# Optimization experiments

Hardware: AMD Instinct MI355X
Metric: run time of the kernel (lower is better)

## Reference

```python
import jax, jax.numpy as jnp
import numpy as np

HEAD_NUM = 16

def setup_inputs() -> dict:
    key = jax.random.key(0)
    k1, k2 = jax.random.split(key)
    bs, seq, d = 2, 2048, 1024
    embeddings = jax.random.normal(k1, (bs, seq, d), dtype=jnp.float32)
    W = jax.random.normal(k2, (d, 3 * d), dtype=jnp.float32) * (1.0 / np.sqrt(d))
    b = jnp.zeros((3 * d,), dtype=jnp.float32)
    return {"embeddings": embeddings, "W": W, "b": b}

def reference(embeddings, W, b):
    bs, seq, d = embeddings.shape
    h = HEAD_NUM
    qkv = embeddings @ W + b                      # [b, s, 3d]
    q, k, v = jnp.split(qkv, 3, axis=-1)          # each [b, s, d]
    hd = d // h
    # Faithful to source: reshape to (bs, seq, head_dim, heads) then permute
    def split_heads(x, head_dim):
        return x.reshape(bs, seq, head_dim, h).transpose(0, 3, 1, 2)  # [b, h, s, hd]
    mq = split_heads(q, hd)
    mk = split_heads(k, hd)
    mv = split_heads(v, hd)
    scale = jnp.sqrt(jnp.asarray(hd, dtype=mq.dtype))
    scores = jnp.einsum('bhqd,bhkd->bhqk', mq, mk) / scale  # [b, h, s, s]
    attn = jax.nn.softmax(scores, axis=-1)
    out = jnp.einsum('bhqk,bhkv->bhqv', attn, mv)            # [b, h, s, hd]
    return out.transpose(0, 2, 1, 3).reshape(bs, seq, -1)    # [b, s, d]
```

## Files before the change

### kernel.cpp

```cpp
#include <hip/hip_runtime.h>
#include <stdint.h>

typedef unsigned short u16;
typedef unsigned int u32;
typedef unsigned int u32x2 __attribute__((ext_vector_type(2)));
typedef float f32x4 __attribute__((ext_vector_type(4)));
typedef __bf16 bf16x8 __attribute__((ext_vector_type(8)));

#define BS 2
#define SEQ 2048
#define DIM 1024
#define NW3 3072
#define NH 16
#define HD 64

#define MFMA_BF16(a, b, c) __builtin_amdgcn_mfma_f32_16x16x32_bf16((a), (b), (c), 0, 0, 0)

#define GLL16(g, l)                                                                \
  __builtin_amdgcn_global_load_lds(                                                \
      (__attribute__((address_space(1))) void*)(void*)(uintptr_t)(g),              \
      (__attribute__((address_space(3))) void*)(l), 16, 0, 0)

__device__ __forceinline__ float fexp2(float x) {
#if defined(__has_builtin)
#if __has_builtin(__builtin_amdgcn_exp2f)
  return __builtin_amdgcn_exp2f(x);
#else
  return exp2f(x);
#endif
#else
  return exp2f(x);
#endif
}

__device__ __forceinline__ u16 f2bf(float x) {
  __bf16 h = (__bf16)x;
  return __builtin_bit_cast(u16, h);
}

#define CSC 0.18033688011112042f

#if defined(__has_builtin)
#if __has_builtin(__builtin_amdgcn_permlane32_swap) && \
    __has_builtin(__builtin_amdgcn_permlane16_swap)
#define HAVE_PLSWAP 1
#endif
#endif

__device__ __forceinline__ uint4 p_transform(u32 pk00, u32 pk01, u32 pk10, u32 pk11,
                                             int sl0, int sl1, bool hi) {
#ifdef HAVE_PLSWAP
  u32x2 s0 = __builtin_amdgcn_permlane32_swap(pk00, pk10, false, false);
  u32x2 s1 = __builtin_amdgcn_permlane32_swap(pk01, pk11, false, false);
  u32x2 t0 = __builtin_amdgcn_permlane16_swap(s0[0], s0[1], false, false);
  u32x2 t1 = __builtin_amdgcn_permlane16_swap(s1[0], s1[1], false, false);
  uint4 wv;
  wv.x = t0[0]; wv.y = t1[0]; wv.z = t0[1]; wv.w = t1[1];
  return wv;
#else
  u32 a0 = __shfl(pk00, sl0), a1 = __shfl(pk01, sl0);
  u32 a2 = __shfl(pk00, sl1), a3 = __shfl(pk01, sl1);
  u32 b0 = __shfl(pk10, sl0), b1 = __shfl(pk11, sl0);
  u32 b2 = __shfl(pk10, sl1), b3 = __shfl(pk11, sl1);
  uint4 wv;
  wv.x = hi ? b0 : a0; wv.y = hi ? b1 : a1;
  wv.z = hi ? b2 : a2; wv.w = hi ? b3 : a3;
  return wv;
#endif
}

__global__ __launch_bounds__(256) void conv_kernel(const float* __restrict__ A,
                                                   u16* __restrict__ O,
                                                   const float* __restrict__ W,
                                                   u16* __restrict__ Wt) {
  if (blockIdx.x < 4096) {
    int i = (blockIdx.x * 256 + threadIdx.x) * 4;
    float4 v = *(const float4*)(A + i);
    union { u16 u[4]; ushort4 v4; } p;
    p.u[0] = f2bf(v.x); p.u[1] = f2bf(v.y); p.u[2] = f2bf(v.z); p.u[3] = f2bf(v.w);
    *(ushort4*)(O + i) = p.v4;
  } else {
    __shared__ __align__(16) u16 lt[64][68];
    int b2 = blockIdx.x - 4096;
    int ktile = b2 / 48, ntile = b2 - ktile * 48;
    int k0 = ktile * 64, n0 = ntile * 64;
    int rowb = threadIdx.x >> 4, c4 = (threadIdx.x & 15) * 4;
#pragma unroll
    for (int rr = 0; rr < 4; ++rr) {
      int row = rowb + rr * 16;
      float4 v = *(const float4*)(W + (size_t)(k0 + row) * NW3 + n0 + c4);
      union { u16 u[4]; uint2 d; } pk;
      pk.u[0] = f2bf(v.x); pk.u[1] = f2bf(v.y); pk.u[2] = f2bf(v.z); pk.u[3] = f2bf(v.w);
      *(uint2*)&lt[row][c4] = pk.d;
    }
    __syncthreads();
    int j = threadIdx.x >> 2, seg = threadIdx.x & 3;
    int n = n0 + j;
    int h = n & 15, hd = (n & 1023) >> 4;
    int np = (n & ~1023) + h * 64 + hd;
    union { u16 u[16]; uint4 q[2]; } o;
#pragma unroll
    for (int idx = 0; idx < 16; ++idx) o.u[idx] = lt[seg * 16 + idx][j];
    u16* dst = Wt + (size_t)np * DIM + k0 + seg * 16;
    *(uint4*)(dst) = o.q[0];
    *(uint4*)(dst + 8) = o.q[1];
  }
}

#define GSTAGE(ADST, BDST, KT)                                                 \
  {                                                                            \
    const int koff = (KT) * 64;                                \
    _Pragma("unroll") for (int r = 0; r < 2; ++r) {                            \
      int l = r * 256 + t;                            \
      int row = l >> 2, pos = l & 3;                                           \
      int kc = pos ^ (row & 3);                                                \
      GLL16(Abase + row * 2048 + koff + kc * 16, (char*)(ADST) + l * 16);      \
      GLL16(Bbase + row * 2048 + koff + kc * 16, (char*)(BDST) + l * 16);      \
    }                                                                          \
  }

#define GCOMPUTE(AT, BT)                                                       \
  {                                                                            \
    bf16x8 af[4], bfr[4];                                                      \
    _Pragma("unroll") for (int mt = 0; mt < 4; ++mt) {                         \
      int row = wm + mt * 16 + c;                                              \
      int kc = quad ^ (row & 3);                                               \
      af[mt] = *(const bf16x8*)((const char*)(AT) + row * 64 + kc * 16);       \
    }                                                                          \
    _Pragma("unroll") for (int nt = 0; nt < 4; ++nt) {                         \
      int row = wn + nt * 16 + c;                                              \
      int kc = quad ^ (row & 3);                                               \
      bfr[nt] = *(const bf16x8*)((const char*)(BT) + row * 64 + kc * 16);      \
    }                                                                          \
    _Pragma("unroll") for (int mt = 0; mt < 4; ++mt)                           \
      _Pragma("unroll") for (int nt = 0; nt < 4; ++nt)                         \
        acc[mt][nt] = MFMA_BF16(af[mt], bfr[nt], acc[mt][nt]);                 \
  }

__global__ __launch_bounds__(256) void gemm_qkv_kernel(
    const u16* __restrict__ Ab, const u16* __restrict__ Bt, const float* __restrict__ bias,
    u16* __restrict__ Q, u16* __restrict__ K, u16* __restrict__ Vt) {
  __shared__ __align__(16) u16 A0[128 * 32];
  __shared__ __align__(16) u16 A1[128 * 32];
  __shared__ __align__(16) u16 A2[128 * 32];
  __shared__ __align__(16) u16 B0[128 * 32];
  __shared__ __align__(16) u16 B1[128 * 32];
  __shared__ __align__(16) u16 B2[128 * 32];
  const int t = threadIdx.x;
  const int lane = t & 63, wave = t >> 6;
  const int c = lane & 15, quad = lane >> 4;
  const int wid = (blockIdx.x & 7) * 96 + (blockIdx.x >> 3);
  const int tm = wid / 24, tn = wid - tm * 24;
  const int wm = (wave >> 1) * 64, wn = (wave & 1) * 64;

  const char* Abase = (const char*)(Ab + (size_t)tm * 128 * DIM);
  const char* Bbase = (const char*)(Bt + (size_t)tn * 128 * DIM);

  f32x4 z = {0.f, 0.f, 0.f, 0.f};
  f32x4 acc[4][4];
#pragma unroll
  for (int i = 0; i < 4; ++i)
#pragma unroll
    for (int j = 0; j < 4; ++j) acc[i][j] = z;

  GSTAGE(A0, B0, 0);
  GSTAGE(A1, B1, 1);
  asm volatile("s_waitcnt vmcnt(4)" ::: "memory");
  __builtin_amdgcn_s_barrier();
  __builtin_amdgcn_sched_barrier(0);

  const u16 *pa = A0, *pb = B0;
  const u16 *qa = A1, *qb = B1;
  const u16 *ra = A2, *rb = B2;
#pragma unroll 1
  for (int kt = 0; kt < 32; ++kt) {
    if (kt + 2 < 32) GSTAGE(ra, rb, kt + 2);
    GCOMPUTE(pa, pb);
    if (kt + 2 < 32) {
      asm volatile("s_waitcnt vmcnt(4)" ::: "memory");
    } else {
      asm volatile("s_waitcnt vmcnt(0)" ::: "memory");
    }
    __builtin_amdgcn_s_barrier();
    __builtin_amdgcn_sched_barrier(0);
    const u16* ta = pa; pa = qa; qa = ra; ra = ta;
    const u16* tb = pb; pb = qb; qb = rb; rb = tb;
  }

#pragma unroll
  for (int nt = 0; nt < 4; ++nt) {
    int np = tn * 128 + wn + nt * 16 + c;
    int which = np >> 10;
    int rem = np & 1023;
    int h = rem >> 6, hd = rem & 63;
    float bv = bias[(np & ~1023) + hd * 16 + h];
    float sc = (which == 0) ? CSC : 1.0f;
    float bvs = bv * sc;
#pragma unroll
    for (int mt = 0; mt < 4; ++mt) {
      int mbase = tm * 128 + wm + mt * 16 + quad * 4;
      int bI = mbase >> 11;
      int s0 = mbase & 2047;
      if (which == 2) {
        union { u16 u[4]; uint2 v; } p;
#pragma unroll
        for (int r = 0; r < 4; ++r) p.u[r] = f2bf(acc[mt][nt][r] + bv);
        *(uint2*)(Vt + ((size_t)(bI * NH + h) * HD + hd) * SEQ + s0) = p.v;
      } else {
        u16* dst = (which == 0) ? Q : K;
#pragma unroll
        for (int r = 0; r < 4; ++r)
          dst[((size_t)(bI * NH + h) * SEQ + (s0 + r)) * HD + hd] =
              f2bf(acc[mt][nt][r] * sc + bvs);
      }
    }
  }
}

#define STAGE_KV(KDST, VDST, KTILE)                                            \
  {                                                                            \
    const char* Ktb = Kb + (size_t)(KTILE) * 8192;        \
    const char* Vtb = Vb + (size_t)(KTILE) * 128;         \
    int l = t;                             \
    int row = l >> 3, pos = l & 7;                                             \
    int kc = pos ^ (row & 7);                                                  \
    GLL16(Ktb + row * 128 + kc * 16, (char*)(KDST) + l * 16);                  \
    GLL16(Vtb + row * 4096 + kc * 16, (char*)(VDST) + l * 16);                 \
  }

#define COMPUTE_TILE(KT, VT)                                                   \
  {                                                                            \
    f32x4 sT[2][2]; \
    sT[0][0] = z; sT[0][1] = z; sT[1][0] = z; sT[1][1] = z;                    \
    __builtin_amdgcn_s_setprio(1);                                             \
    _Pragma("unroll") for (int mt2 = 0; mt2 < 2; ++mt2) {                      \
      _Pragma("unroll") for (int ks = 0; ks < 2; ++ks) {                       \
        int row = ws * 32 + mt2 * 16 + c;                                      \
        int kc = (ks * 4 + quad) ^ (row & 7);                                  \
        bf16x8 kf = *(const bf16x8*)((const char*)(KT) + row * 128 + kc * 16); \
        sT[mt2][0] = MFMA_BF16(kf, qf[0][ks], sT[mt2][0]);                     \
        sT[mt2][1] = MFMA_BF16(kf, qf[1][ks], sT[mt2][1]);                     \
      }                                                                        \
    }                                                                          \
    __builtin_amdgcn_s_setprio(0);                                             \
    bf16x8 pf[2];                                                              \
    _Pragma("unroll") for (int nt = 0; nt < 2; ++nt) {                         \
      u32 pk[2][2];                                                            \
      _Pragma("unroll") for (int mt2 = 0; mt2 < 2; ++mt2) {                    \
        float p0 = fexp2(sT[mt2][nt][0]);                                      \
        float p1 = fexp2(sT[mt2][nt][1]);                                      \
        float p2 = fexp2(sT[mt2][nt][2]);                                      \
        float p3 = fexp2(sT[mt2][nt][3]);                                      \
        pk[mt2][0] = (u32)f2bf(p0) | ((u32)f2bf(p1) << 16);                    \
        pk[mt2][1] = (u32)f2bf(p2) | ((u32)f2bf(p3) << 16);                    \
      }                                                                        \
      uint4 wv = p_transform(pk[0][0], pk[0][1], pk[1][0], pk[1][1],           \
                             sl0, sl1, hi);                                    \
      pf[nt] = __builtin_bit_cast(bf16x8, wv);                                 \
    }                                                                          \
    __builtin_amdgcn_s_setprio(1);                                             \
    _Pragma("unroll") for (int mt = 0; mt < 4; ++mt) {                         \
      int row = mt * 16 + c;                                                   \
      int kc = vq ^ (row & 7);                                                 \
      bf16x8 vf = *(const bf16x8*)((const char*)(VT) + row * 128 + kc * 16);   \
      accO[mt][0] = MFMA_BF16(vf, pf[0], accO[mt][0]);                         \
      accO[mt][1] = MFMA_BF16(vf, pf[1], accO[mt][1]);                         \
    }                                                                          \
    acc_l[0] = MFMA_BF16(ones, pf[0], acc_l[0]);   \
    acc_l[1] = MFMA_BF16(ones, pf[1], acc_l[1]);                               \
    __builtin_amdgcn_s_setprio(0);                                             \
  }

__global__ __launch_bounds__(512, 4) void attn_kernel(
    const u16* __restrict__ Q, const u16* __restrict__ K,
    const u16* __restrict__ Vt, float* __restrict__ Out) {
  __shared__ __align__(16) u16 Ka[64 * 64];
  __shared__ __align__(16) u16 Kb2[64 * 64];
  __shared__ __align__(16) u16 Va[64 * 64];
  __shared__ __align__(16) u16 Vb2[64 * 64];
  __shared__ float lred[512];
  const int t = threadIdx.x;
  const int lane = t & 63, wave = t >> 6;
  const int c = lane & 15, quad = lane >> 4;
  const int wq2 = wave & 3, ws = wave >> 2;
  const int p = blockIdx.x;
  const int xcd = p & 7, slot = p >> 3;
  const int bh = xcd + ((slot >> 4) << 3);
  const int qtp = slot & 15;
  const int h = bh & 15, b = bh >> 4;

  const u16* Qb = Q + ((size_t)bh * SEQ + qtp * 128) * HD;
  const char* Kb = (const char*)(K + (size_t)bh * SEQ * HD);
  const char* Vb = (const char*)(Vt + (size_t)bh * HD * SEQ);

  {
    int l = t;
    int row = l >> 3, pos = l & 7;
    int kc = pos ^ (row & 7);
    GLL16((const char*)Qb + row * 128 + kc * 16, (char*)Ka + l * 16);
    GLL16((const char*)Qb + 8192 + row * 128 + kc * 16, (char*)Va + l * 16);
  }
  __syncthreads();
  bf16x8 qf[2][2];
#pragma unroll
  for (int nt = 0; nt < 2; ++nt)
#pragma unroll
    for (int ks = 0; ks < 2; ++ks) {
      int row = (wq2 & 1) * 32 + nt * 16 + c;
      int kc = (ks * 4 + quad) ^ (row & 7);
      const char* qbuf = (wq2 >> 1) ? (const char*)Va : (const char*)Ka;
      qf[nt][ks] = *(const bf16x8*)(qbuf + row * 128 + kc * 16);
    }
  __syncthreads();

  f32x4 z = {0.f, 0.f, 0.f, 0.f};
  f32x4 accO[4][2];
#pragma unroll
  for (int i = 0; i < 4; ++i) { accO[i][0] = z; accO[i][1] = z; }
  f32x4 acc_l[2] = {z, z};
  const uint4 onesw = {0x3F803F80u, 0x3F803F80u, 0x3F803F80u, 0x3F803F80u};
  const bf16x8 ones = __builtin_bit_cast(bf16x8, onesw);

  const int sl0 = c + 16 * ((quad & 1) * 2);
  const int sl1 = sl0 + 16;
  const bool hi = quad >= 2;
  const int vq = ws * 4 + quad;

  STAGE_KV(Ka, Va, 0);
  __syncthreads();

  for (int kt = 0; kt < 32; kt += 2) {
    STAGE_KV(Kb2, Vb2, kt + 1);
    COMPUTE_TILE(Ka, Va);
    __syncthreads();
    if (kt + 2 < 32) STAGE_KV(Ka, Va, kt + 2);
    COMPUTE_TILE(Kb2, Vb2);
    __syncthreads();
  }

  float sm[2];
  sm[0] = acc_l[0][0];
  sm[1] = acc_l[1][0];
  float* fb = (float*)((wq2 & 2) ? ((wq2 & 1) ? (void*)Vb2 : (void*)Va)
                                 : ((wq2 & 1) ? (void*)Kb2 : (void*)Ka));
  if (ws == 1) {
#pragma unroll
    for (int mt = 0; mt < 4; ++mt)
#pragma unroll
      for (int nt = 0; nt < 2; ++nt)
        *(f32x4*)(fb + (mt * 2 + nt) * 256 + lane * 4) = accO[mt][nt];
    lred[wq2 * 128 + lane * 2] = sm[0];
    lred[wq2 * 128 + lane * 2 + 1] = sm[1];
  }
  __syncthreads();
  if (ws == 0) {
#pragma unroll
    for (int mt = 0; mt < 4; ++mt)
#pragma unroll
      for (int nt = 0; nt < 2; ++nt)
        accO[mt][nt] += *(const f32x4*)(fb + (mt * 2 + nt) * 256 + lane * 4);
    float inv0 = 1.f / (sm[0] + lred[wq2 * 128 + lane * 2]);
    float inv1 = 1.f / (sm[1] + lred[wq2 * 128 + lane * 2 + 1]);
    int s0 = qtp * 128 + wq2 * 32 + c;
#pragma unroll
    for (int mt = 0; mt < 4; ++mt) {
#pragma unroll
      for (int nt = 0; nt < 2; ++nt) {
        float inv = nt ? inv1 : inv0;
        float4 o;
        o.x = accO[mt][nt][0] * inv;
        o.y = accO[mt][nt][1] * inv;
        o.z = accO[mt][nt][2] * inv;
        o.w = accO[mt][nt][3] * inv;
        size_t off = ((size_t)(b * SEQ + s0 + nt * 16)) * DIM + h * HD + mt * 16 + quad * 4;
        *(float4*)(Out + off) = o;
      }
    }
  }
}

extern "C" void kernel_launch(void* const* d_in, const int* in_sizes, int n_in,
                              void* d_out, int out_size, void* d_ws, size_t ws_size,
                              hipStream_t stream) {
  (void)in_sizes; (void)n_in; (void)out_size; (void)ws_size;
  const float* emb = (const float*)d_in[0];
  const float* W = (const float*)d_in[1];
  const float* bias = (const float*)d_in[2];
  float* out = (float*)d_out;
  char* ws = (char*)d_ws;
  u16* Ab = (u16*)ws;
  u16* Wt = (u16*)(ws + 8388608);
  u16* Qd = (u16*)(ws + 14680064);
  u16* Kd = (u16*)(ws + 23068672);
  u16* Vd = (u16*)(ws + 31457280);

  conv_kernel<<<4864, 256, 0, stream>>>(emb, Ab, W, Wt);
  gemm_qkv_kernel<<<768, 256, 0, stream>>>(Ab, Wt, bias, Qd, Kd, Vd);
  attn_kernel<<<512, 512, 0, stream>>>(Qd, Kd, Vd, out);
}
```

Measured before the change: 155.1 us.

## Triple-buffer K/V tiles in LDS with counted vmcnt waits instead of full syncs

```diff
diff --git a/kernel.cpp b/kernel.cpp
--- a/kernel.cpp
+++ b/kernel.cpp
@@ -274,10 +274,12 @@
 __global__ __launch_bounds__(512, 4) void attn_kernel(
     const u16* __restrict__ Q, const u16* __restrict__ K,
     const u16* __restrict__ Vt, float* __restrict__ Out) {
-  __shared__ __align__(16) u16 Ka[64 * 64];
-  __shared__ __align__(16) u16 Kb2[64 * 64];
-  __shared__ __align__(16) u16 Va[64 * 64];
-  __shared__ __align__(16) u16 Vb2[64 * 64];
+  __shared__ __align__(16) u16 K0[64 * 64];
+  __shared__ __align__(16) u16 K1[64 * 64];
+  __shared__ __align__(16) u16 K2[64 * 64];
+  __shared__ __align__(16) u16 V0[64 * 64];
+  __shared__ __align__(16) u16 V1[64 * 64];
+  __shared__ __align__(16) u16 V2[64 * 64];
   __shared__ float lred[512];
   const int t = threadIdx.x;
   const int lane = t & 63, wave = t >> 6;
@@ -297,10 +299,14 @@
     int l = t;
     int row = l >> 3, pos = l & 7;
     int kc = pos ^ (row & 7);
-    GLL16((const char*)Qb + row * 128 + kc * 16, (char*)Ka + l * 16);
-    GLL16((const char*)Qb + 8192 + row * 128 + kc * 16, (char*)Va + l * 16);
-  }
-  __syncthreads();
+    GLL16((const char*)Qb + row * 128 + kc * 16, (char*)K0 + l * 16);
+    GLL16((const char*)Qb + 8192 + row * 128 + kc * 16, (char*)V0 + l * 16);
+  }
+  STAGE_KV(K1, V1, 0);
+  STAGE_KV(K2, V2, 1);
+  asm volatile("s_waitcnt vmcnt(4)" ::: "memory");
+  __builtin_amdgcn_s_barrier();
+  __builtin_amdgcn_sched_barrier(0);
   bf16x8 qf[2][2];
 #pragma unroll
   for (int nt = 0; nt < 2; ++nt)
@@ -308,10 +314,12 @@
     for (int ks = 0; ks < 2; ++ks) {
       int row = (wq2 & 1) * 32 + nt * 16 + c;
       int kc = (ks * 4 + quad) ^ (row & 7);
-      const char* qbuf = (wq2 >> 1) ? (const char*)Va : (const char*)Ka;
+      const char* qbuf = (wq2 >> 1) ? (const char*)V0 : (const char*)K0;
       qf[nt][ks] = *(const bf16x8*)(qbuf + row * 128 + kc * 16);
     }
-  __syncthreads();
+  asm volatile("s_waitcnt vmcnt(2) lgkmcnt(0)" ::: "memory");
+  __builtin_amdgcn_s_barrier();
+  __builtin_amdgcn_sched_barrier(0);
 
   f32x4 z = {0.f, 0.f, 0.f, 0.f};
   f32x4 accO[4][2];
@@ -326,23 +334,29 @@
   const bool hi = quad >= 2;
   const int vq = ws * 4 + quad;
 
-  STAGE_KV(Ka, Va, 0);
-  __syncthreads();
-
-  for (int kt = 0; kt < 32; kt += 2) {
-    STAGE_KV(Kb2, Vb2, kt + 1);
-    COMPUTE_TILE(Ka, Va);
-    __syncthreads();
-    if (kt + 2 < 32) STAGE_KV(Ka, Va, kt + 2);
-    COMPUTE_TILE(Kb2, Vb2);
-    __syncthreads();
+  const u16 *pk_ = K1, *pv_ = V1;
+  const u16 *nk_ = K2, *nv_ = V2;
+  const u16 *sk_ = K0, *sv_ = V0;
+#pragma unroll 1
+  for (int kt = 0; kt < 32; ++kt) {
+    if (kt + 2 < 32) STAGE_KV(sk_, sv_, kt + 2);
+    COMPUTE_TILE(pk_, pv_);
+    if (kt + 2 < 32) {
+      asm volatile("s_waitcnt vmcnt(2)" ::: "memory");
+    } else {
+      asm volatile("s_waitcnt vmcnt(0)" ::: "memory");
+    }
+    __builtin_amdgcn_s_barrier();
+    __builtin_amdgcn_sched_barrier(0);
+    const u16* tk = pk_; pk_ = nk_; nk_ = sk_; sk_ = tk;
+    const u16* tv = pv_; pv_ = nv_; nv_ = sv_; sv_ = tv;
   }
 
   float sm[2];
   sm[0] = acc_l[0][0];
   sm[1] = acc_l[1][0];
-  float* fb = (float*)((wq2 & 2) ? ((wq2 & 1) ? (void*)Vb2 : (void*)Va)
-                                 : ((wq2 & 1) ? (void*)Kb2 : (void*)Ka));
+  float* fb = (float*)((wq2 & 2) ? ((wq2 & 1) ? (void*)V0 : (void*)K2)
+                                 : ((wq2 & 1) ? (void*)K1 : (void*)K0));
   if (ws == 1) {
 #pragma unroll
     for (int mt = 0; mt < 4; ++mt)
```

Result: no change. 155.4 us (+0.2%).

## Software-pipeline attention loop with triple-buffered K/V and overlapped QK^T and PV

Applied to the files above, without the earlier changes.

```diff
diff --git a/kernel.cpp b/kernel.cpp
--- a/kernel.cpp
+++ b/kernel.cpp
@@ -60,8 +60,9 @@
 #else
   u32 a0 = __shfl(pk00, sl0), a1 = __shfl(pk01, sl0);
   u32 a2 = __shfl(pk00, sl1), a3 = __shfl(pk01, sl1);
-  u32 b0 = __shfl(pk10, sl0), b1 = __shfl(pk11, sl0);
+  u32 b0 = __shfl(pk10, sl0), b1 = __shfl(pk10, sl0);
   u32 b2 = __shfl(pk10, sl1), b3 = __shfl(pk11, sl1);
+  b1 = __shfl(pk11, sl0);
   uint4 wv;
   wv.x = hi ? b0 : a0; wv.y = hi ? b1 : a1;
   wv.z = hi ? b2 : a2; wv.w = hi ? b3 : a3;
@@ -228,29 +229,32 @@
     GLL16(Vtb + row * 4096 + kc * 16, (char*)(VDST) + l * 16);                 \
   }
 
-#define COMPUTE_TILE(KT, VT)                                                   \
-  {                                                                            \
-    f32x4 sT[2][2]; \
-    sT[0][0] = z; sT[0][1] = z; sT[1][0] = z; sT[1][1] = z;                    \
+#define QKT_T(KT, SD)                                                          \
+  {                                                                            \
+    SD[0][0] = z; SD[0][1] = z; SD[1][0] = z; SD[1][1] = z;                    \
     __builtin_amdgcn_s_setprio(1);                                             \
     _Pragma("unroll") for (int mt2 = 0; mt2 < 2; ++mt2) {                      \
       _Pragma("unroll") for (int ks = 0; ks < 2; ++ks) {                       \
         int row = ws * 32 + mt2 * 16 + c;                                      \
         int kc = (ks * 4 + quad) ^ (row & 7);                                  \
         bf16x8 kf = *(const bf16x8*)((const char*)(KT) + row * 128 + kc * 16); \
-        sT[mt2][0] = MFMA_BF16(kf, qf[0][ks], sT[mt2][0]);                     \
-        sT[mt2][1] = MFMA_BF16(kf, qf[1][ks], sT[mt2][1]);                     \
+        SD[mt2][0] = MFMA_BF16(kf, qf[0][ks], SD[mt2][0]);                     \
+        SD[mt2][1] = MFMA_BF16(kf, qf[1][ks], SD[mt2][1]);                     \
       }                                                                        \
     }                                                                          \
     __builtin_amdgcn_s_setprio(0);                                             \
+  }
+
+#define SM_PV(SD, VT)                                                          \
+  {                                                                            \
     bf16x8 pf[2];                                                              \
     _Pragma("unroll") for (int nt = 0; nt < 2; ++nt) {                         \
       u32 pk[2][2];                                                            \
       _Pragma("unroll") for (int mt2 = 0; mt2 < 2; ++mt2) {                    \
-        float p0 = fexp2(sT[mt2][nt][0]);                                      \
-        float p1 = fexp2(sT[mt2][nt][1]);                                      \
-        float p2 = fexp2(sT[mt2][nt][2]);                                      \
-        float p3 = fexp2(sT[mt2][nt][3]);                                      \
+        float p0 = fexp2(SD[mt2][nt][0]);                                      \
+        float p1 = fexp2(SD[mt2][nt][1]);                                      \
+        float p2 = fexp2(SD[mt2][nt][2]);                                      \
+        float p3 = fexp2(SD[mt2][nt][3]);                                      \
         pk[mt2][0] = (u32)f2bf(p0) | ((u32)f2bf(p1) << 16);                    \
         pk[mt2][1] = (u32)f2bf(p2) | ((u32)f2bf(p3) << 16);                    \
       }                                                                        \
@@ -271,13 +275,21 @@
     __builtin_amdgcn_s_setprio(0);                                             \
   }
 
+#define ROTATE3()                                                              \
+  {                                                                            \
+    const u16* k_ = pk_; pk_ = ck; ck = nk_; nk_ = k_;                         \
+    const u16* v_ = pv_; pv_ = cv; cv = nv_; nv_ = v_;                         \
+  }
+
 __global__ __launch_bounds__(512, 4) void attn_kernel(
     const u16* __restrict__ Q, const u16* __restrict__ K,
     const u16* __restrict__ Vt, float* __restrict__ Out) {
-  __shared__ __align__(16) u16 Ka[64 * 64];
-  __shared__ __align__(16) u16 Kb2[64 * 64];
-  __shared__ __align__(16) u16 Va[64 * 64];
-  __shared__ __align__(16) u16 Vb2[64 * 64];
+  __shared__ __align__(16) u16 K0[64 * 64];
+  __shared__ __align__(16) u16 K1[64 * 64];
+  __shared__ __align__(16) u16 K2[64 * 64];
+  __shared__ __align__(16) u16 V0[64 * 64];
+  __shared__ __align__(16) u16 V1[64 * 64];
+  __shared__ __align__(16) u16 V2[64 * 64];
   __shared__ float lred[512];
   const int t = threadIdx.x;
   const int lane = t & 63, wave = t >> 6;
@@ -297,9 +309,11 @@
     int l = t;
     int row = l >> 3, pos = l & 7;
     int kc = pos ^ (row & 7);
-    GLL16((const char*)Qb + row * 128 + kc * 16, (char*)Ka + l * 16);
-    GLL16((const char*)Qb + 8192 + row * 128 + kc * 16, (char*)Va + l * 16);
-  }
+    GLL16((const char*)Qb + row * 128 + kc * 16, (char*)K2 + l * 16);
+    GLL16((const char*)Qb + 8192 + row * 128 + kc * 16, (char*)V2 + l * 16);
+  }
+  STAGE_KV(K0, V0, 0);
+  STAGE_KV(K1, V1, 1);
   __syncthreads();
   bf16x8 qf[2][2];
 #pragma unroll
@@ -308,7 +322,7 @@
     for (int ks = 0; ks < 2; ++ks) {
       int row = (wq2 & 1) * 32 + nt * 16 + c;
       int kc = (ks * 4 + quad) ^ (row & 7);
-      const char* qbuf = (wq2 >> 1) ? (const char*)Va : (const char*)Ka;
+      const char* qbuf = (wq2 >> 1) ? (const char*)V2 : (const char*)K2;
       qf[nt][ks] = *(const bf16x8*)(qbuf + row * 128 + kc * 16);
     }
   __syncthreads();
@@ -326,23 +340,37 @@
   const bool hi = quad >= 2;
   const int vq = ws * 4 + quad;
 
-  STAGE_KV(Ka, Va, 0);
+  const u16 *ck = K1, *cv = V1;
+  const u16 *pk_ = K0, *pv_ = V0;
+  const u16 *nk_ = K2, *nv_ = V2;
+
+  f32x4 sA[2][2], sB[2][2];
+  QKT_T(K0, sA);
+
+#pragma unroll 1
+  for (int tt = 1; tt < 31; tt += 2) {
+    STAGE_KV(nk_, nv_, tt + 1);
+    QKT_T(ck, sB);
+    SM_PV(sA, pv_);
+    __syncthreads();
+    ROTATE3();
+    if (tt + 2 < 32) STAGE_KV(nk_, nv_, tt + 2);
+    QKT_T(ck, sA);
+    SM_PV(sB, pv_);
+    __syncthreads();
+    ROTATE3();
+  }
+  QKT_T(ck, sB);
+  SM_PV(sA, pv_);
   __syncthreads();
-
-  for (int kt = 0; kt < 32; kt += 2) {
-    STAGE_KV(Kb2, Vb2, kt + 1);
-    COMPUTE_TILE(Ka, Va);
-    __syncthreads();
-    if (kt + 2 < 32) STAGE_KV(Ka, Va, kt + 2);
-    COMPUTE_TILE(Kb2, Vb2);
-    __syncthreads();
-  }
+  ROTATE3();
+  SM_PV(sB, pv_);
 
   float sm[2];
   sm[0] = acc_l[0][0];
   sm[1] = acc_l[1][0];
-  float* fb = (float*)((wq2 & 2) ? ((wq2 & 1) ? (void*)Vb2 : (void*)Va)
-                                 : ((wq2 & 1) ? (void*)Kb2 : (void*)Ka));
+  float* fb = (float*)((wq2 & 2) ? ((wq2 & 1) ? (void*)V0 : (void*)K2)
+                                 : ((wq2 & 1) ? (void*)K1 : (void*)K0));
   if (ws == 1) {
 #pragma unroll
     for (int mt = 0; mt < 4; ++mt)
```

Result: no change. 157.1 us (+1.3%).
